# Performance work log

Hardware: AMD Instinct MI355X
Metric: run time of the kernel (lower is better)

The kernel has to match this reference:

```python
import jax, jax.numpy as jnp
import numpy as np

B, N, D, H, P = 16, 1024, 768, 12, 16
HD = D // H
FF = 4 * D
SCALE = HD ** -0.5


def _layer_norm(x, g, b, eps=1e-5):
    mu = jnp.mean(x, axis=-1, keepdims=True)
    var = jnp.var(x, axis=-1, keepdims=True)
    return (x - mu) * jax.lax.rsqrt(var + eps) * g + b


def setup_inputs() -> dict:
    key = jax.random.key(0)
    ks = jax.random.split(key, 8)
    s = 0.02
    return {
        "x": jax.random.normal(ks[0], (B, N, D), jnp.float32),
        "prompt": jax.random.normal(ks[1], (B, 2, P, H, HD), jnp.float32),
        "qkv_w": jax.random.normal(ks[2], (3 * D, D), jnp.float32) * s,
        "qkv_b": jnp.zeros((3 * D,), jnp.float32),
        "out_w": jax.random.normal(ks[3], (D, D), jnp.float32) * s,
        "out_b": jnp.zeros((D,), jnp.float32),
        "ln1_g": jnp.ones((D,), jnp.float32),
        "ln1_b": jnp.zeros((D,), jnp.float32),
        "ln2_g": jnp.ones((D,), jnp.float32),
        "ln2_b": jnp.zeros((D,), jnp.float32),
        "fc1_w": jax.random.normal(ks[4], (FF, D), jnp.float32) * s,
        "fc1_b": jnp.zeros((FF,), jnp.float32),
        "fc2_w": jax.random.normal(ks[5], (D, FF), jnp.float32) * s,
        "fc2_b": jnp.zeros((D,), jnp.float32),
    }


def reference(x, prompt, qkv_w, qkv_b, out_w, out_b, ln1_g, ln1_b,
              ln2_g, ln2_b, fc1_w, fc1_b, fc2_w, fc2_b):
    # --- attention branch ---
    h = _layer_norm(x, ln1_g, ln1_b)                       # [B,N,D]
    qkv = h @ qkv_w.T + qkv_b                              # [B,N,3D]
    qkv = qkv.reshape(B, N, 3, H, HD).transpose(2, 0, 3, 1, 4)  # [3,B,H,N,hd]
    q, k, v = qkv[0], qkv[1], qkv[2]
    # prompt [B,2,P,H,hd] -> [2,B,H,P,hd]
    pr = jnp.transpose(prompt, (1, 0, 3, 2, 4))
    k = jnp.concatenate([pr[0], k], axis=2)                # [B,H,P+N,hd]
    v = jnp.concatenate([pr[1], v], axis=2)
    attn = jnp.einsum("bhqd,bhkd->bhqk", q, k) * SCALE     # [B,H,N,P+N]
    attn = jax.nn.softmax(attn, axis=-1)
    o = jnp.einsum("bhqk,bhkd->bhqd", attn, v)             # [B,H,N,hd]
    o = o.transpose(0, 2, 1, 3).reshape(B, N, D)
    o = o @ out_w.T + out_b
    x = x + o
    # --- MLP branch (CLIP: c_fc -> QuickGELU -> c_proj) ---
    h2 = _layer_norm(x, ln2_g, ln2_b)
    m = h2 @ fc1_w.T + fc1_b
    m = m * jax.nn.sigmoid(1.702 * m)                      # QuickGELU
    m = m @ fc2_w.T + fc2_b
    return x + m
```

## Files before the change

### kernel.cpp

```cpp
#include <hip/hip_runtime.h>
#include <hip/hip_bf16.h>

typedef __bf16 bf16;
typedef __attribute__((ext_vector_type(8))) __bf16 bf16x8;
typedef __attribute__((ext_vector_type(4))) __bf16 bf16x4;
typedef __attribute__((ext_vector_type(4))) float f32x4;

#define GLOBAL_AS __attribute__((address_space(1)))
#define LDS_AS __attribute__((address_space(3)))

constexpr int B_  = 16;
constexpr int N_  = 1024;
constexpr int D_  = 768;
constexpr int H_  = 12;
constexpr int P_  = 16;
constexpr int FF_ = 3072;
constexpr int BN_ = B_ * N_;
constexpr int LP_ = 1088;
constexpr float EXPC_ = 0.18033688f;

__global__ __launch_bounds__(256) void cvt_kernel(
    const float* __restrict__ s0, const float* __restrict__ s1,
    const float* __restrict__ s2, const float* __restrict__ s3,
    bf16* __restrict__ d0, bf16* __restrict__ d1,
    bf16* __restrict__ d2, bf16* __restrict__ d3)
{
    int i = (blockIdx.x * 256 + threadIdx.x) * 4;
    const float* s; bf16* d; int off;
    if (i < 1769472)      { s = s0; d = d0; off = i; }
    else if (i < 2359296) { s = s1; d = d1; off = i - 1769472; }
    else if (i < 4718592) { s = s2; d = d2; off = i - 2359296; }
    else                  { s = s3; d = d3; off = i - 4718592; }
    float4 f = *(const float4*)(s + off);
    bf16x4 o;
    o[0] = (bf16)f.x; o[1] = (bf16)f.y; o[2] = (bf16)f.z; o[3] = (bf16)f.w;
    *(bf16x4*)(d + off) = o;
}

__global__ __launch_bounds__(256) void prep_kernel(
    const float* __restrict__ prompt, bf16* __restrict__ Kall,
    bf16* __restrict__ VTall)
{
    int hb = blockIdx.x;
    int b = hb / 12, h = hb % 12;
    int t = threadIdx.x;
    size_t kbase = (size_t)hb * LP_ * 64;
    size_t vbase = (size_t)hb * 64 * LP_;

    {
        int p = t >> 4, d0 = (t & 15) * 4;
        const float* src = prompt + (((size_t)(b * 2 + 0) * P_ + p) * H_ + h) * 64 + d0;
        float4 f = *(const float4*)src;
        bf16x4 o4;
        o4[0] = (bf16)f.x; o4[1] = (bf16)f.y; o4[2] = (bf16)f.z; o4[3] = (bf16)f.w;
        *(bf16x4*)(Kall + kbase + (size_t)p * 64 + d0) = o4;
    }
    {
        int d = t >> 2, p0 = (t & 3) * 4;
        bf16x4 o4;
#pragma unroll
        for (int j = 0; j < 4; j++)
            o4[j] = (bf16)prompt[(((size_t)(b * 2 + 1) * P_ + p0 + j) * H_ + h) * 64 + d];
        *(bf16x4*)(VTall + vbase + (size_t)d * LP_ + p0) = o4;
    }
    {
        bf16* kp = Kall + kbase + 1040 * 64 + (size_t)t * 12;
#pragma unroll
        for (int i = 0; i < 12; i++) kp[i] = (bf16)0.f;
        int d = t >> 2, j0 = (t & 3) * 12;
        bf16* vp = VTall + vbase + (size_t)d * LP_ + 1040 + j0;
#pragma unroll
        for (int i = 0; i < 12; i++) vp[i] = (bf16)0.f;
    }
}

__global__ __launch_bounds__(256) void ln_kernel(
    const float* __restrict__ x, const float* __restrict__ g,
    const float* __restrict__ bta, bf16* __restrict__ out)
{
    int row = blockIdx.x;
    const float* xr = x + (size_t)row * D_;
    int t = threadIdx.x;
    float v[3];
    float s = 0.f, ss = 0.f;
#pragma unroll
    for (int i = 0; i < 3; i++) {
        v[i] = xr[t + i * 256];
        s += v[i];
        ss += v[i] * v[i];
    }
#pragma unroll
    for (int o = 32; o > 0; o >>= 1) {
        s  += __shfl_down(s, o);
        ss += __shfl_down(ss, o);
    }
    __shared__ float red_s[4], red_ss[4];
    int w = t >> 6, lane = t & 63;
    if (lane == 0) { red_s[w] = s; red_ss[w] = ss; }
    __syncthreads();
    s  = red_s[0] + red_s[1] + red_s[2] + red_s[3];
    ss = red_ss[0] + red_ss[1] + red_ss[2] + red_ss[3];
    float mu = s * (1.f / 768.f);
    float var = ss * (1.f / 768.f) - mu * mu;
    float rstd = rsqrtf(var + 1e-5f);
#pragma unroll
    for (int i = 0; i < 3; i++) {
        int c = t + i * 256;
        out[(size_t)row * D_ + c] = (bf16)((v[i] - mu) * rstd * g[c] + bta[c]);
    }
}

template <int EPI>
__global__ __launch_bounds__(256, 2) void gemm_bt(
    const bf16* __restrict__ A, const bf16* __restrict__ Bt,
    const float* __restrict__ bias, const float* __restrict__ res,
    float* __restrict__ outF, bf16* __restrict__ outB,
    bf16* __restrict__ Qall, bf16* __restrict__ Kall, bf16* __restrict__ VTall,
    int M, int N, int K)
{
    __shared__ bf16 As[128 * 32];
    __shared__ bf16 Bs[128 * 32];

    const int tid = threadIdx.x;
    const int w = tid >> 6, lane = tid & 63;
    const int wr = w >> 1, wc = w & 1;
    const int lrow = lane & 15, khalf = lane >> 4;
    const int rowBase = blockIdx.y * 128;
    const int colBase = blockIdx.x * 128;

    f32x4 acc[4][4];
#pragma unroll
    for (int mi = 0; mi < 4; mi++)
#pragma unroll
        for (int ni = 0; ni < 4; ni++)
            acc[mi][ni] = (f32x4){0.f, 0.f, 0.f, 0.f};

    for (int k0 = 0; k0 < K; k0 += 32) {
#pragma unroll
        for (int i = 0; i < 2; i++) {
            int idx = w * 128 + i * 64 + lane;
            int r = idx >> 2, c = idx & 3;
            int cs = c ^ ((r >> 1) & 3);
            __builtin_amdgcn_global_load_lds(
                (const GLOBAL_AS void*)(A + (size_t)(rowBase + r) * K + k0 + cs * 8),
                (LDS_AS void*)(As + (size_t)(w * 128 + i * 64) * 8), 16, 0, 0);
        }
#pragma unroll
        for (int i = 0; i < 2; i++) {
            int idx = w * 128 + i * 64 + lane;
            int r = idx >> 2, c = idx & 3;
            int cs = c ^ ((r >> 1) & 3);
            __builtin_amdgcn_global_load_lds(
                (const GLOBAL_AS void*)(Bt + (size_t)(colBase + r) * K + k0 + cs * 8),
                (LDS_AS void*)(Bs + (size_t)(w * 128 + i * 64) * 8), 16, 0, 0);
        }
        __syncthreads();

        bf16x8 af[4], bfr[4];
#pragma unroll
        for (int mi = 0; mi < 4; mi++) {
            int rr = wr * 64 + mi * 16 + lrow;
            af[mi] = *(const bf16x8*)(As + (size_t)rr * 32 + ((khalf ^ ((rr >> 1) & 3)) * 8));
        }
#pragma unroll
        for (int ni = 0; ni < 4; ni++) {
            int rr = wc * 64 + ni * 16 + lrow;
            bfr[ni] = *(const bf16x8*)(Bs + (size_t)rr * 32 + ((khalf ^ ((rr >> 1) & 3)) * 8));
        }
#pragma unroll
        for (int mi = 0; mi < 4; mi++)
#pragma unroll
            for (int ni = 0; ni < 4; ni++)
                acc[mi][ni] = __builtin_amdgcn_mfma_f32_16x16x32_bf16(
                    af[mi], bfr[ni], acc[mi][ni], 0, 0, 0);
        __syncthreads();
    }

#pragma unroll
    for (int mi = 0; mi < 4; mi++) {
#pragma unroll
        for (int ni = 0; ni < 4; ni++) {
            int col = colBase + wc * 64 + ni * 16 + lrow;
            int row0 = rowBase + wr * 64 + mi * 16 + khalf * 4;
            float bv = bias[col];
            if constexpr (EPI == 3) {
                int sect = (col >= 1536) ? 2 : (col >= 768 ? 1 : 0);
                int hh = (col >> 6) - sect * 12;
                int dd = col & 63;
                int bb = row0 >> 10, n0 = row0 & 1023;
                size_t bh = (size_t)bb * 12 + hh;
                if (sect == 0) {
                    bf16* qp = Qall + (bh * 1024 + n0) * 64 + dd;
#pragma unroll
                    for (int r = 0; r < 4; r++)
                        qp[(size_t)r * 64] = (bf16)(acc[mi][ni][r] + bv);
                } else if (sect == 1) {
                    bf16* kp = Kall + bh * (LP_ * 64) + (size_t)(16 + n0) * 64 + dd;
#pragma unroll
                    for (int r = 0; r < 4; r++)
                        kp[(size_t)r * 64] = (bf16)(acc[mi][ni][r] + bv);
                } else {
                    bf16x4 pv;
#pragma unroll
                    for (int r = 0; r < 4; r++)
                        pv[r] = (bf16)(acc[mi][ni][r] + bv);
                    *(bf16x4*)(VTall + bh * (64 * LP_) + (size_t)dd * LP_ + 16 + n0) = pv;
                }
            } else {
#pragma unroll
                for (int r = 0; r < 4; r++) {
                    size_t idx = (size_t)(row0 + r) * N + col;
                    float v = acc[mi][ni][r] + bv;
                    if constexpr (EPI == 1) {
                        outF[idx] = v + res[idx];
                    } else {
                        outB[idx] = (bf16)(v / (1.f + __expf(-1.702f * v)));
                    }
                }
            }
        }
    }
}

__global__ __launch_bounds__(256, 2) void attn_kernel(
    const bf16* __restrict__ Qall, const bf16* __restrict__ Kall,
    const bf16* __restrict__ VTall, bf16* __restrict__ o)
{
    __shared__ bf16 Qs[128 * 64];
    __shared__ bf16 Ks[64 * 64];
    __shared__ bf16 Vt[64 * 64];
    __shared__ bf16 Ps[4 * 32 * 72];

    const int lid = blockIdx.x;
    const int xcd = lid & 7, slot = lid >> 3;
    const int hb = xcd * 24 + (slot >> 3);
    const int qt = slot & 7;
    const int h = hb % 12, b = hb / 12;

    const int tid = threadIdx.x;
    const int w = tid >> 6, lane = tid & 63;
    const int lrow = lane & 15, q4 = lane >> 4;

    const bf16* qb = Qall + ((size_t)hb * 1024 + qt * 128) * 64;
#pragma unroll
    for (int i = 0; i < 4; i++) {
        int idx = i * 256 + w * 64 + lane;
        int r = idx >> 3, c = idx & 7, cs = c ^ (r & 7);
        __builtin_amdgcn_global_load_lds(
            (const GLOBAL_AS void*)(qb + (size_t)r * 64 + cs * 8),
            (LDS_AS void*)(Qs + (size_t)idx * 8), 16, 0, 0);
    }

    f32x4 acc_o[2][4];
    float lp[2][4];
#pragma unroll
    for (int mi = 0; mi < 2; mi++) {
#pragma unroll
        for (int ni = 0; ni < 4; ni++) acc_o[mi][ni] = (f32x4){0.f, 0.f, 0.f, 0.f};
#pragma unroll
        for (int r = 0; r < 4; r++) lp[mi][r] = 0.f;
    }

    const bf16* kb = Kall + (size_t)hb * LP_ * 64;
    const bf16* vb = VTall + (size_t)hb * 64 * LP_;
    bf16* pw = Ps + w * (32 * 72);

    for (int kt = 0; kt < 17; kt++) {
        __syncthreads();
#pragma unroll
        for (int i = 0; i < 2; i++) {
            int idx = w * 128 + i * 64 + lane;
            int r = idx >> 3, c = idx & 7, cs = c ^ (r & 7);
            __builtin_amdgcn_global_load_lds(
                (const GLOBAL_AS void*)(kb + (size_t)kt * 4096 + (size_t)r * 64 + cs * 8),
                (LDS_AS void*)(Ks + (size_t)idx * 8), 16, 0, 0);
        }
#pragma unroll
        for (int i = 0; i < 2; i++) {
            int idx = w * 128 + i * 64 + lane;
            int r = idx >> 3, c = idx & 7, cs = c ^ (r & 7);
            __builtin_amdgcn_global_load_lds(
                (const GLOBAL_AS void*)(vb + (size_t)r * LP_ + kt * 64 + cs * 8),
                (LDS_AS void*)(Vt + (size_t)idx * 8), 16, 0, 0);
        }
        __syncthreads();

        const int ntile = (kt == 16) ? 1 : 4;
        f32x4 accs[2][4];
#pragma unroll
        for (int mi = 0; mi < 2; mi++)
#pragma unroll
            for (int ni = 0; ni < 4; ni++) accs[mi][ni] = (f32x4){0.f, 0.f, 0.f, 0.f};

#pragma unroll
        for (int ks = 0; ks < 2; ks++) {
            bf16x8 qf[2];
#pragma unroll
            for (int mi = 0; mi < 2; mi++) {
                int rr = w * 32 + mi * 16 + lrow;
                int ch = ks * 4 + q4;
                qf[mi] = *(const bf16x8*)(Qs + (size_t)rr * 64 + ((ch ^ (rr & 7)) * 8));
            }
#pragma unroll
            for (int ni = 0; ni < 4; ni++) {
                if (ni >= ntile) continue;
                int rr = ni * 16 + lrow;
                int ch = ks * 4 + q4;
                bf16x8 kf = *(const bf16x8*)(Ks + (size_t)rr * 64 + ((ch ^ (rr & 7)) * 8));
                accs[0][ni] = __builtin_amdgcn_mfma_f32_16x16x32_bf16(qf[0], kf, accs[0][ni], 0, 0, 0);
                accs[1][ni] = __builtin_amdgcn_mfma_f32_16x16x32_bf16(qf[1], kf, accs[1][ni], 0, 0, 0);
            }
        }

#pragma unroll
        for (int mi = 0; mi < 2; mi++) {
#pragma unroll
            for (int r = 0; r < 4; r++) {
                int prow = mi * 16 + q4 * 4 + r;
                float psum = 0.f;
#pragma unroll
                for (int ni = 0; ni < 4; ni++) {
                    float p = (kt == 16 && ni > 0) ? 0.f
                              : exp2f(accs[mi][ni][r] * EXPC_);
                    pw[(size_t)prow * 72 + ni * 16 + lrow] = (bf16)p;
                    psum += p;
                }
                lp[mi][r] += psum;
            }
        }

#pragma unroll
        for (int ks = 0; ks < 2; ks++) {
            bf16x8 pf[2];
#pragma unroll
            for (int mi = 0; mi < 2; mi++)
                pf[mi] = *(const bf16x8*)(pw + (size_t)(mi * 16 + lrow) * 72 + ks * 32 + q4 * 8);
#pragma unroll
            for (int ni = 0; ni < 4; ni++) {
                bf16x8 vf = *(const bf16x8*)(Vt + (size_t)(ni * 16 + lrow) * 64 +
                                             (((ks * 4 + q4) ^ ((ni * 16 + lrow) & 7)) * 8));
                acc_o[0][ni] = __builtin_amdgcn_mfma_f32_16x16x32_bf16(pf[0], vf, acc_o[0][ni], 0, 0, 0);
                acc_o[1][ni] = __builtin_amdgcn_mfma_f32_16x16x32_bf16(pf[1], vf, acc_o[1][ni], 0, 0, 0);
            }
        }
    }

    float linv[2][4];
#pragma unroll
    for (int mi = 0; mi < 2; mi++)
#pragma unroll
        for (int r = 0; r < 4; r++) {
            float ls = lp[mi][r];
#pragma unroll
            for (int sft = 1; sft < 16; sft <<= 1) ls += __shfl_xor(ls, sft);
            linv[mi][r] = 1.f / ls;
        }

    bf16* ob = o + (size_t)(b * N_ + qt * 128 + w * 32) * 768 + h * 64;
#pragma unroll
    for (int mi = 0; mi < 2; mi++)
#pragma unroll
        for (int ni = 0; ni < 4; ni++)
#pragma unroll
            for (int r = 0; r < 4; r++) {
                int row = mi * 16 + q4 * 4 + r;
                ob[(size_t)row * 768 + ni * 16 + lrow] =
                    (bf16)(acc_o[mi][ni][r] * linv[mi][r]);
            }
}

extern "C" void kernel_launch(void* const* d_in, const int* in_sizes, int n_in,
                              void* d_out, int out_size, void* d_ws, size_t ws_size,
                              hipStream_t stream)
{
    const float* x      = (const float*)d_in[0];
    const float* prompt = (const float*)d_in[1];
    const float* qkv_w  = (const float*)d_in[2];
    const float* qkv_b  = (const float*)d_in[3];
    const float* out_w  = (const float*)d_in[4];
    const float* out_b  = (const float*)d_in[5];
    const float* ln1_g  = (const float*)d_in[6];
    const float* ln1_b  = (const float*)d_in[7];
    const float* ln2_g  = (const float*)d_in[8];
    const float* ln2_b  = (const float*)d_in[9];
    const float* fc1_w  = (const float*)d_in[10];
    const float* fc1_b  = (const float*)d_in[11];
    const float* fc2_w  = (const float*)d_in[12];
    const float* fc2_b  = (const float*)d_in[13];
    float* out = (float*)d_out;

    bf16* qkvw_b = (bf16*)d_ws;
    bf16* outw_b = qkvw_b + 1769472;
    bf16* fc1w_b = outw_b + 589824;
    bf16* fc2w_b = fc1w_b + 2359296;
    bf16* h_b    = fc2w_b + 2359296;
    bf16* o_b    = h_b    + 12582912;
    bf16* Qall   = o_b    + 12582912;
    bf16* Kall   = Qall   + 12582912;
    bf16* VTall  = Kall   + 13369344;
    bf16* mid    = o_b;
    float* x1    = (float*)(VTall + 13369344);

    cvt_kernel<<<6912, 256, 0, stream>>>(qkv_w, out_w, fc1_w, fc2_w,
                                         qkvw_b, outw_b, fc1w_b, fc2w_b);
    prep_kernel<<<192, 256, 0, stream>>>(prompt, Kall, VTall);
    ln_kernel<<<BN_, 256, 0, stream>>>(x, ln1_g, ln1_b, h_b);
    gemm_bt<3><<<dim3(18, 128), 256, 0, stream>>>(h_b, qkvw_b, qkv_b, nullptr,
                                                  nullptr, nullptr, Qall, Kall, VTall,
                                                  BN_, 2304, 768);
    attn_kernel<<<1536, 256, 0, stream>>>(Qall, Kall, VTall, o_b);
    gemm_bt<1><<<dim3(6, 128), 256, 0, stream>>>(o_b, outw_b, out_b, x,
                                                 x1, nullptr, nullptr, nullptr, nullptr,
                                                 BN_, 768, 768);
    ln_kernel<<<BN_, 256, 0, stream>>>(x1, ln2_g, ln2_b, h_b);
    gemm_bt<2><<<dim3(24, 128), 256, 0, stream>>>(h_b, fc1w_b, fc1_b, nullptr,
                                                  nullptr, mid, nullptr, nullptr, nullptr,
                                                  BN_, FF_, 768);
    gemm_bt<1><<<dim3(6, 128), 256, 0, stream>>>(mid, fc2w_b, fc2_b, x1,
                                                 out, nullptr, nullptr, nullptr, nullptr,
                                                 BN_, 768, FF_);
}
```

Measured before the change: 611.2 us.

## Double GEMM K-tile to 64 and store residual stream in bf16

The GEMM K-step grows from 32 to 64, with a new XOR swizzle over 8 chunks, so each barrier pair covers two MFMA sub-steps and the loop synchronises half as often. The intermediate residual x1 is now stored in bf16 instead of fp32, which halves its write and its two later reads (LN2 and the fc2 residual add). LDS use per block doubles, which may affect occupancy. Keeping the residual in bf16 also loses precision on the skip path.

```diff
diff --git a/kernel.cpp b/kernel.cpp
--- a/kernel.cpp
+++ b/kernel.cpp
@@ -74,18 +74,19 @@
     }
 }
 
+template <typename T>
 __global__ __launch_bounds__(256) void ln_kernel(
-    const float* __restrict__ x, const float* __restrict__ g,
+    const T* __restrict__ x, const float* __restrict__ g,
     const float* __restrict__ bta, bf16* __restrict__ out)
 {
     int row = blockIdx.x;
-    const float* xr = x + (size_t)row * D_;
+    const T* xr = x + (size_t)row * D_;
     int t = threadIdx.x;
     float v[3];
     float s = 0.f, ss = 0.f;
 #pragma unroll
     for (int i = 0; i < 3; i++) {
-        v[i] = xr[t + i * 256];
+        v[i] = (float)xr[t + i * 256];
         s += v[i];
         ss += v[i] * v[i];
     }
@@ -113,13 +114,14 @@
 template <int EPI>
 __global__ __launch_bounds__(256, 2) void gemm_bt(
     const bf16* __restrict__ A, const bf16* __restrict__ Bt,
-    const float* __restrict__ bias, const float* __restrict__ res,
+    const float* __restrict__ bias,
+    const float* __restrict__ resF, const bf16* __restrict__ resB,
     float* __restrict__ outF, bf16* __restrict__ outB,
     bf16* __restrict__ Qall, bf16* __restrict__ Kall, bf16* __restrict__ VTall,
     int M, int N, int K)
 {
-    __shared__ bf16 As[128 * 32];
-    __shared__ bf16 Bs[128 * 32];
+    __shared__ bf16 As[128 * 64];
+    __shared__ bf16 Bs[128 * 64];
 
     const int tid = threadIdx.x;
     const int w = tid >> 6, lane = tid & 63;
@@ -135,44 +137,49 @@
         for (int ni = 0; ni < 4; ni++)
             acc[mi][ni] = (f32x4){0.f, 0.f, 0.f, 0.f};
 
-    for (int k0 = 0; k0 < K; k0 += 32) {
-#pragma unroll
-        for (int i = 0; i < 2; i++) {
-            int idx = w * 128 + i * 64 + lane;
-            int r = idx >> 2, c = idx & 3;
-            int cs = c ^ ((r >> 1) & 3);
+    for (int k0 = 0; k0 < K; k0 += 64) {
+#pragma unroll
+        for (int i = 0; i < 4; i++) {
+            int idx = i * 256 + w * 64 + lane;
+            int r = idx >> 3, c = idx & 7;
+            int cs = c ^ (r & 7);
             __builtin_amdgcn_global_load_lds(
                 (const GLOBAL_AS void*)(A + (size_t)(rowBase + r) * K + k0 + cs * 8),
-                (LDS_AS void*)(As + (size_t)(w * 128 + i * 64) * 8), 16, 0, 0);
-        }
-#pragma unroll
-        for (int i = 0; i < 2; i++) {
-            int idx = w * 128 + i * 64 + lane;
-            int r = idx >> 2, c = idx & 3;
-            int cs = c ^ ((r >> 1) & 3);
+                (LDS_AS void*)(As + (size_t)idx * 8), 16, 0, 0);
+        }
+#pragma unroll
+        for (int i = 0; i < 4; i++) {
+            int idx = i * 256 + w * 64 + lane;
+            int r = idx >> 3, c = idx & 7;
+            int cs = c ^ (r & 7);
             __builtin_amdgcn_global_load_lds(
                 (const GLOBAL_AS void*)(Bt + (size_t)(colBase + r) * K + k0 + cs * 8),
-                (LDS_AS void*)(Bs + (size_t)(w * 128 + i * 64) * 8), 16, 0, 0);
+                (LDS_AS void*)(Bs + (size_t)idx * 8), 16, 0, 0);
         }
         __syncthreads();
 
-        bf16x8 af[4], bfr[4];
-#pragma unroll
-        for (int mi = 0; mi < 4; mi++) {
-            int rr = wr * 64 + mi * 16 + lrow;
-            af[mi] = *(const bf16x8*)(As + (size_t)rr * 32 + ((khalf ^ ((rr >> 1) & 3)) * 8));
-        }
-#pragma unroll
-        for (int ni = 0; ni < 4; ni++) {
-            int rr = wc * 64 + ni * 16 + lrow;
-            bfr[ni] = *(const bf16x8*)(Bs + (size_t)rr * 32 + ((khalf ^ ((rr >> 1) & 3)) * 8));
-        }
-#pragma unroll
-        for (int mi = 0; mi < 4; mi++)
-#pragma unroll
-            for (int ni = 0; ni < 4; ni++)
-                acc[mi][ni] = __builtin_amdgcn_mfma_f32_16x16x32_bf16(
-                    af[mi], bfr[ni], acc[mi][ni], 0, 0, 0);
+#pragma unroll
+        for (int ks = 0; ks < 2; ks++) {
+            bf16x8 af[4], bfr[4];
+#pragma unroll
+            for (int mi = 0; mi < 4; mi++) {
+                int rr = wr * 64 + mi * 16 + lrow;
+                int ch = (ks * 4 + khalf) ^ (rr & 7);
+                af[mi] = *(const bf16x8*)(As + (size_t)rr * 64 + ch * 8);
+            }
+#pragma unroll
+            for (int ni = 0; ni < 4; ni++) {
+                int rr = wc * 64 + ni * 16 + lrow;
+                int ch = (ks * 4 + khalf) ^ (rr & 7);
+                bfr[ni] = *(const bf16x8*)(Bs + (size_t)rr * 64 + ch * 8);
+            }
+#pragma unroll
+            for (int mi = 0; mi < 4; mi++)
+#pragma unroll
+                for (int ni = 0; ni < 4; ni++)
+                    acc[mi][ni] = __builtin_amdgcn_mfma_f32_16x16x32_bf16(
+                        af[mi], bfr[ni], acc[mi][ni], 0, 0, 0);
+        }
         __syncthreads();
     }
 
@@ -212,9 +219,11 @@
                     size_t idx = (size_t)(row0 + r) * N + col;
                     float v = acc[mi][ni][r] + bv;
                     if constexpr (EPI == 1) {
-                        outF[idx] = v + res[idx];
+                        outF[idx] = v + (float)resB[idx];
+                    } else if constexpr (EPI == 2) {
+                        outB[idx] = (bf16)(v / (1.f + __expf(-1.702f * v)));
                     } else {
-                        outB[idx] = (bf16)(v / (1.f + __expf(-1.702f * v)));
+                        outB[idx] = (bf16)(v + resF[idx]);
                     }
                 }
             }
@@ -399,24 +408,24 @@
     bf16* Kall   = Qall   + 12582912;
     bf16* VTall  = Kall   + 13369344;
     bf16* mid    = o_b;
-    float* x1    = (float*)(VTall + 13369344);
+    bf16* x1b    = VTall + 13369344;
 
     cvt_kernel<<<6912, 256, 0, stream>>>(qkv_w, out_w, fc1_w, fc2_w,
                                          qkvw_b, outw_b, fc1w_b, fc2w_b);
     prep_kernel<<<192, 256, 0, stream>>>(prompt, Kall, VTall);
-    ln_kernel<<<BN_, 256, 0, stream>>>(x, ln1_g, ln1_b, h_b);
-    gemm_bt<3><<<dim3(18, 128), 256, 0, stream>>>(h_b, qkvw_b, qkv_b, nullptr,
+    ln_kernel<float><<<BN_, 256, 0, stream>>>(x, ln1_g, ln1_b, h_b);
+    gemm_bt<3><<<dim3(18, 128), 256, 0, stream>>>(h_b, qkvw_b, qkv_b, nullptr, nullptr,
                                                   nullptr, nullptr, Qall, Kall, VTall,
                                                   BN_, 2304, 768);
     attn_kernel<<<1536, 256, 0, stream>>>(Qall, Kall, VTall, o_b);
-    gemm_bt<1><<<dim3(6, 128), 256, 0, stream>>>(o_b, outw_b, out_b, x,
-                                                 x1, nullptr, nullptr, nullptr, nullptr,
+    gemm_bt<4><<<dim3(6, 128), 256, 0, stream>>>(o_b, outw_b, out_b, x, nullptr,
+                                                 nullptr, x1b, nullptr, nullptr, nullptr,
                                                  BN_, 768, 768);
-    ln_kernel<<<BN_, 256, 0, stream>>>(x1, ln2_g, ln2_b, h_b);
-    gemm_bt<2><<<dim3(24, 128), 256, 0, stream>>>(h_b, fc1w_b, fc1_b, nullptr,
+    ln_kernel<bf16><<<BN_, 256, 0, stream>>>(x1b, ln2_g, ln2_b, h_b);
+    gemm_bt<2><<<dim3(24, 128), 256, 0, stream>>>(h_b, fc1w_b, fc1_b, nullptr, nullptr,
                                                   nullptr, mid, nullptr, nullptr, nullptr,
                                                   BN_, FF_, 768);
-    gemm_bt<1><<<dim3(6, 128), 256, 0, stream>>>(mid, fc2w_b, fc2_b, x1,
+    gemm_bt<1><<<dim3(6, 128), 256, 0, stream>>>(mid, fc2w_b, fc2_b, nullptr, x1b,
                                                  out, nullptr, nullptr, nullptr, nullptr,
                                                  BN_, 768, FF_);
 }
```

After: 571.8 us. -6.4%, faster.
